# Kernel optimization log

Measured on AMD Instinct MI355X. Metric: run time of the kernel, lower is better.

Reference implementation:

```python
import jax, jax.numpy as jnp
import numpy as np

# ---- static config (mirrors GptOssDecoderLayer init) ----
H = 1024      # hidden_size
HD = 64       # head_size
NQ = 16       # num_query_heads
NKV = 4       # num_key_value_heads
G = NQ // NKV # num_key_value_groups
E = 8         # num_experts
TOPK = 2      # experts_per_token
FFN = 1024    # expert intermediate (== hidden in GPT-OSS)
B, Q = 4, 128 # batch sequences, new query tokens per sequence
P, PS = 8, 128
S = P * PS    # kv length per sequence
T = B * Q     # total query tokens
SW = 128      # sliding window (layer_idx % 2 == 0 -> active)
LIMIT = 7.0   # swiglu_limit
ALPHA = 1.702
EPS = 1e-5
NEG = -1e30
SCALE = HD ** -0.5


def rmsnorm(x, w):
    return x * w * jax.lax.rsqrt(jnp.mean(x * x, axis=-1, keepdims=True) + EPS)


def setup_inputs() -> dict:
    key = jax.random.key(0)
    ks = jax.random.split(key, 16)
    hidden = jax.random.normal(ks[0], (T, H), jnp.float32)
    kv_cache = jax.random.normal(ks[1], (B * P, 2, PS, NKV, HD), jnp.float32)
    kv_page_indices = jnp.arange(B * P, dtype=jnp.int32).reshape(B, P)
    # additive causal mask: query q sits at absolute position S - Q + q
    qpos = S - Q + jnp.arange(Q)
    kpos = jnp.arange(S)
    causal = qpos[:, None] >= kpos[None, :]
    attention_mask = jnp.broadcast_to(
        jnp.where(causal, 0.0, NEG).astype(jnp.float32), (B, Q, S))
    sinks = 0.1 * jax.random.normal(ks[2], (NQ,), jnp.float32)
    w_qkv = jax.random.normal(ks[3], (H, HD * (NQ + 2 * NKV)), jnp.float32) / np.sqrt(H)
    b_qkv = jnp.zeros((HD * (NQ + 2 * NKV),), jnp.float32)
    w_o = jax.random.normal(ks[4], (NQ * HD, H), jnp.float32) / np.sqrt(NQ * HD)
    b_o = jnp.zeros((H,), jnp.float32)
    ln1_w = jnp.ones((H,), jnp.float32)
    ln2_w = jnp.ones((H,), jnp.float32)
    w_router = jax.random.normal(ks[5], (H, E), jnp.float32) / np.sqrt(H)
    b_router = jnp.zeros((E,), jnp.float32)
    w_gate_up = jax.random.normal(ks[6], (E, H, 2 * FFN), jnp.float32) / np.sqrt(H)
    b_gate_up = jnp.zeros((E, 2 * FFN), jnp.float32)
    w_down = jax.random.normal(ks[7], (E, FFN, H), jnp.float32) / np.sqrt(FFN)
    b_down = jnp.zeros((E, H), jnp.float32)
    return dict(hidden=hidden, kv_cache=kv_cache, attention_mask=attention_mask,
                kv_page_indices=kv_page_indices, sinks=sinks, w_qkv=w_qkv,
                b_qkv=b_qkv, w_o=w_o, b_o=b_o, ln1_w=ln1_w, ln2_w=ln2_w,
                w_router=w_router, b_router=b_router, w_gate_up=w_gate_up,
                b_gate_up=b_gate_up, w_down=w_down, b_down=b_down)


def reference(hidden, kv_cache, attention_mask, kv_page_indices, sinks,
              w_qkv, b_qkv, w_o, b_o, ln1_w, ln2_w, w_router, b_router,
              w_gate_up, b_gate_up, w_down, b_down):
    # ---- attention block ----
    x = rmsnorm(hidden, ln1_w)
    qkv = x @ w_qkv + b_qkv                       # [T, HD*(NQ+2*NKV)]
    q = qkv[:, :NQ * HD].reshape(B, Q, NQ, HD)
    k_new = qkv[:, NQ * HD:(NQ + NKV) * HD].reshape(B, Q, NKV, HD)
    v_new = qkv[:, (NQ + NKV) * HD:].reshape(B, Q, NKV, HD)
    # gather paged KV cache -> [B, S, NKV, HD]; write new tokens into tail slots
    pages = kv_cache[kv_page_indices]             # [B, P, 2, PS, NKV, HD]
    K = pages[:, :, 0].reshape(B, S, NKV, HD).at[:, S - Q:].set(k_new)
    V = pages[:, :, 1].reshape(B, S, NKV, HD).at[:, S - Q:].set(v_new)
    Kr = jnp.repeat(K, G, axis=2)                 # GQA expand -> [B, S, NQ, HD]
    Vr = jnp.repeat(V, G, axis=2)
    scores = jnp.einsum('bqhd,bshd->bhqs', q * SCALE, Kr) + attention_mask[:, None]
    # sliding-window (module trims pages outside the window; equivalent mask)
    qpos = S - Q + jnp.arange(Q)
    kpos = jnp.arange(S)
    win_ok = (qpos[:, None] - kpos[None, :]) < SW
    scores = jnp.where(win_ok[None, None], scores, NEG)
    m = jnp.max(scores, axis=-1)
    m = jnp.where(jnp.isinf(m) & (m < 0), 0.0, m)
    p = jnp.exp(scores - m[..., None])            # [B, NQ, Q, S]
    # attention sink joins the softmax denominator (online-softmax correction)
    denom = jnp.sum(p, axis=-1) + jnp.exp(sinks[None, :, None] - m)
    attn = jnp.einsum('bhqs,bshd->bhqd', p, Vr) / denom[..., None]
    attn = attn.transpose(0, 2, 1, 3).reshape(T, NQ * HD)
    h = hidden + attn @ w_o + b_o
    # ---- MoE block ----
    x2 = rmsnorm(h, ln2_w)
    logits = x2 @ w_router + b_router             # [T, E]
    vals, idx = jax.lax.top_k(logits, TOPK)
    wts = jax.nn.softmax(vals, axis=-1)
    comb = jnp.sum(jax.nn.one_hot(idx, E, dtype=x2.dtype) * wts[..., None], axis=1)
    gu = jnp.einsum('th,ehf->etf', x2, w_gate_up) + b_gate_up[:, None, :]
    gate = jnp.minimum(gu[..., 0::2], LIMIT)
    up = jnp.clip(gu[..., 1::2], -LIMIT, LIMIT)
    glu = gate * jax.nn.sigmoid(gate * ALPHA)
    eo = jnp.einsum('etf,efh->eth', (up + 1.0) * glu, w_down) + b_down[:, None, :]
    moe = jnp.einsum('te,eth->th', comb, eo)
    return h + moe
```

## Files before the change

### kernel.cpp

```cpp
#include <hip/hip_runtime.h>

constexpr int H    = 1024;
constexpr int HD   = 64;
constexpr int NQ   = 16;
constexpr int NKV  = 4;
constexpr int E_   = 8;
constexpr int FFN  = 1024;
constexpr int B_   = 4;
constexpr int Q_   = 128;
constexpr int P_   = 8;
constexpr int PS   = 128;
constexpr int S_   = P_ * PS;
constexpr int T_   = B_ * Q_;
constexpr int QKV_N = HD * (NQ + 2 * NKV);
constexpr float EPS   = 1e-5f;
constexpr float ALPHA = 1.702f;
constexpr float LIMIT = 7.0f;
constexpr float SCALE = 0.125f;

constexpr int MAXROWS = 1536;

typedef __attribute__((ext_vector_type(4))) float f32x4;
typedef __attribute__((ext_vector_type(8))) short s16x8;

__device__ __forceinline__ unsigned short f2bf(float f) {
    unsigned u = __float_as_uint(f);
    u += 0x7FFFu + ((u >> 16) & 1u);
    return (unsigned short)(u >> 16);
}

__global__ __launch_bounds__(256) void repack_all_kernel(const float* __restrict__ wgu,
                                                         const float* __restrict__ wdn,
                                                         const float* __restrict__ wqkv,
                                                         const float* __restrict__ wo,
                                                         unsigned short* __restrict__ g,
                                                         unsigned short* __restrict__ u,
                                                         unsigned short* __restrict__ d,
                                                         unsigned short* __restrict__ q,
                                                         unsigned short* __restrict__ o,
                                                         int* __restrict__ cnt) {
    int idx = blockIdx.x;
    int tid = threadIdx.x;
    if (idx == 0 && tid < E_) cnt[tid] = 0;
    int lane = tid & 63;
    int kq = lane >> 4, c16 = lane & 15;
    if (idx < 4096) {
        int e = idx >> 9, rem = idx & 511;
        int nb = rem >> 3, kb = (rem & 7) * 4 + (tid >> 6);
        const float* s = wgu + ((size_t)e * 1024 + kb * 32 + kq * 8) * 2048 + 2 * (nb * 16 + c16);
        s16x8 pg, pu;
#pragma unroll
        for (int j = 0; j < 8; j++) {
            float2 v = *(const float2*)(s + (size_t)j * 2048);
            pg[j] = (short)f2bf(v.x);
            pu[j] = (short)f2bf(v.y);
        }
        size_t off = ((((size_t)e * 64 + nb) * 32 + kb) * 64 + lane) * 8;
        *(s16x8*)(g + off) = pg;
        *(s16x8*)(u + off) = pu;
    } else if (idx < 8192) {
        int i2 = idx - 4096;
        int e = i2 >> 9, rem = i2 & 511;
        int nb = rem >> 3, kb = (rem & 7) * 4 + (tid >> 6);
        const float* s = wdn + (size_t)e * FFN * H + (size_t)(kb * 32 + kq * 8) * 1024 + nb * 16 + c16;
        s16x8 p;
#pragma unroll
        for (int j = 0; j < 8; j++) p[j] = (short)f2bf(s[(size_t)j * 1024]);
        size_t off = (size_t)e * (64 * 32 * 64 * 8) + (((size_t)nb * 32 + kb) * 64 + lane) * 8;
        *(s16x8*)(d + off) = p;
    } else if (idx < 8960) {
        int i2 = idx - 8192;
        int nb = i2 >> 3, kb = (i2 & 7) * 4 + (tid >> 6);
        const float* s = wqkv + (size_t)(kb * 32 + kq * 8) * QKV_N + nb * 16 + c16;
        s16x8 p;
#pragma unroll
        for (int j = 0; j < 8; j++) p[j] = (short)f2bf(s[(size_t)j * QKV_N]);
        *(s16x8*)(q + (((size_t)nb * 32 + kb) * 64 + lane) * 8) = p;
    } else {
        int i2 = idx - 8960;
        int nb = i2 >> 3, kb = (i2 & 7) * 4 + (tid >> 6);
        const float* s = wo + (size_t)(kb * 32 + kq * 8) * H + nb * 16 + c16;
        s16x8 p;
#pragma unroll
        for (int j = 0; j < 8; j++) p[j] = (short)f2bf(s[(size_t)j * H]);
        *(s16x8*)(o + (((size_t)nb * 32 + kb) * 64 + lane) * 8) = p;
    }
}

__global__ __launch_bounds__(256) void rmsnorm_kernel(const float* __restrict__ in,
                                                      const float* __restrict__ w,
                                                      unsigned short* __restrict__ outb) {
    int t   = blockIdx.x;
    int tid = threadIdx.x;
    float4 v = ((const float4*)(in + (size_t)t * H))[tid];
    float ss = v.x * v.x + v.y * v.y + v.z * v.z + v.w * v.w;
#pragma unroll
    for (int off = 32; off; off >>= 1) ss += __shfl_down(ss, off);
    __shared__ float partial[4];
    __shared__ float s_inv;
    if ((tid & 63) == 0) partial[tid >> 6] = ss;
    __syncthreads();
    if (tid == 0)
        s_inv = rsqrtf((partial[0] + partial[1] + partial[2] + partial[3]) * (1.0f / H) + EPS);
    __syncthreads();
    float inv = s_inv;
    float4 wv = ((const float4*)w)[tid];
    ushort4 ob;
    ob.x = f2bf(v.x * wv.x * inv); ob.y = f2bf(v.y * wv.y * inv);
    ob.z = f2bf(v.z * wv.z * inv); ob.w = f2bf(v.w * wv.w * inv);
    ((ushort4*)(outb + (size_t)t * H))[tid] = ob;
}

__global__ __launch_bounds__(256) void gemm_splitk_bf16(const unsigned short* __restrict__ Abf,
                                                        const unsigned short* __restrict__ Bp,
                                                        const float* __restrict__ bias,
                                                        const float* __restrict__ resid,
                                                        float* __restrict__ C,
                                                        float* __restrict__ Cdup, int N) {
    int tid = threadIdx.x;
    int wv = tid >> 6, lane = tid & 63;
    int nb16 = blockIdx.x, mb = blockIdx.y * 64;
    int r16 = lane & 15, kq = lane >> 4;
    const unsigned short* ap = Abf + (size_t)(mb + r16) * 1024 + wv * 256 + kq * 8;
    const unsigned short* bp = Bp + (((size_t)nb16 * 32 + wv * 8) * 64 + lane) * 8;
    f32x4 acc[4] = {};
#pragma unroll 4
    for (int s = 0; s < 8; s++) {
        s16x8 af[4];
#pragma unroll
        for (int mt = 0; mt < 4; mt++)
            af[mt] = *(const s16x8*)(ap + mt * 16 * 1024 + s * 32);
        s16x8 bf = *(const s16x8*)(bp + s * 512);
#pragma unroll
        for (int mt = 0; mt < 4; mt++)
            acc[mt] = __builtin_amdgcn_mfma_f32_16x16x32_bf16(af[mt], bf, acc[mt], 0, 0, 0);
    }
    __shared__ float red[4][4][4][64];
#pragma unroll
    for (int mt = 0; mt < 4; mt++)
#pragma unroll
        for (int r = 0; r < 4; r++) red[wv][mt][r][lane] = acc[mt][r];
    __syncthreads();
    int mt = tid >> 6, li = tid & 63;
    int kq2 = li >> 4, c16 = li & 15;
    int col = nb16 * 16 + c16;
    float bcol = bias[col];
#pragma unroll
    for (int r = 0; r < 4; r++) {
        float s = red[0][mt][r][li] + red[1][mt][r][li] + red[2][mt][r][li] + red[3][mt][r][li];
        int row = mb + mt * 16 + kq2 * 4 + r;
        float v = s + bcol;
        if (resid) v += resid[(size_t)row * N + col];
        C[(size_t)row * N + col] = v;
        if (Cdup) Cdup[(size_t)row * N + col] = v;
    }
}

__global__ __launch_bounds__(256) void attn_group_kernel(const float* __restrict__ qkv,
                                                         const float* __restrict__ kv_cache,
                                                         const int* __restrict__ page_idx,
                                                         const float* __restrict__ sinks,
                                                         unsigned short* __restrict__ attn_bf) {
    int blk = blockIdx.x;
    int kvh = blk & 3;
    int q   = (blk >> 2) & 127;
    int b   = blk >> 9;
    int t   = b * Q_ + q;
    int tid = threadIdx.x;
    int s_lo = S_ - Q_ - 127 + q;

    __shared__ __align__(16) float Vs[128][64];
    __shared__ __align__(16) float qs4[4][64];
    __shared__ float pv[4][128];
    __shared__ float sD[4];

#pragma unroll
    for (int r = 0; r < 8; r++) {
        int l = r * 256 + tid;
        int key = l >> 4, c = l & 15;
        int s = s_lo + key;
        const float* vp;
        if (s < S_ - Q_) {
            int page = page_idx[b * P_ + (s >> 7)];
            vp = kv_cache + (size_t)page * 65536 + 32768 + (size_t)(s & 127) * (NKV * HD) + kvh * HD;
        } else {
            vp = qkv + (size_t)(b * Q_ + (s - (S_ - Q_))) * QKV_N + (NQ + NKV) * HD + kvh * HD;
        }
        ((float4*)Vs[key])[c] = *(const float4*)(vp + c * 4);
    }
    {
        int hh = tid >> 6, d2 = tid & 63;
        qs4[hh][d2] = qkv[(size_t)t * QKV_N + (kvh * 4 + hh) * HD + d2];
    }
    __syncthreads();

    {
        int key = tid & 127, hp = tid >> 7;
        int s = s_lo + key;
        const float* kp;
        if (s < S_ - Q_) {
            int page = page_idx[b * P_ + (s >> 7)];
            kp = kv_cache + (size_t)page * 65536 + (size_t)(s & 127) * (NKV * HD) + kvh * HD;
        } else {
            kp = qkv + (size_t)(b * Q_ + (s - (S_ - Q_))) * QKV_N + NQ * HD + kvh * HD;
        }
        const float4* kp4 = (const float4*)kp;
        const float4* q0p = (const float4*)qs4[hp * 2];
        const float4* q1p = (const float4*)qs4[hp * 2 + 1];
        float sc0 = 0.f, sc1 = 0.f;
#pragma unroll
        for (int d4 = 0; d4 < 16; d4++) {
            float4 kk = kp4[d4];
            float4 q0 = q0p[d4], q1 = q1p[d4];
            sc0 += q0.x * kk.x + q0.y * kk.y + q0.z * kk.z + q0.w * kk.w;
            sc1 += q1.x * kk.x + q1.y * kk.y + q1.z * kk.z + q1.w * kk.w;
        }
        pv[hp * 2][key]     = sc0 * SCALE;
        pv[hp * 2 + 1][key] = sc1 * SCALE;
    }
    __syncthreads();

    {
        int wv = tid >> 6, lane = tid & 63;
        float a0 = pv[wv][lane], a1 = pv[wv][lane + 64];
        float m = fmaxf(a0, a1);
#pragma unroll
        for (int off = 32; off; off >>= 1) m = fmaxf(m, __shfl_xor(m, off));
        float p0 = __expf(a0 - m), p1 = __expf(a1 - m);
        float l = p0 + p1;
#pragma unroll
        for (int off = 32; off; off >>= 1) l += __shfl_xor(l, off);
        pv[wv][lane] = p0;
        pv[wv][lane + 64] = p1;
        if (lane == 0) sD[wv] = l + __expf(sinks[kvh * 4 + wv] - m);
    }
    __syncthreads();

    {
        int hh = tid >> 6, d2 = tid & 63;
        float a0 = 0.f, a1 = 0.f, a2 = 0.f, a3 = 0.f;
#pragma unroll 4
        for (int i = 0; i < 128; i += 4) {
            a0 += pv[hh][i]     * Vs[i][d2];
            a1 += pv[hh][i + 1] * Vs[i + 1][d2];
            a2 += pv[hh][i + 2] * Vs[i + 2][d2];
            a3 += pv[hh][i + 3] * Vs[i + 3][d2];
        }
        float acc = ((a0 + a1) + (a2 + a3)) / sD[hh];
        attn_bf[(size_t)t * (NQ * HD) + (kvh * 4 + hh) * HD + d2] = f2bf(acc);
    }
}

__global__ __launch_bounds__(256) void rms_router_kernel(const float* __restrict__ hbuf,
                                                         const float* __restrict__ ln2w,
                                                         const float* __restrict__ w_router,
                                                         const float* __restrict__ b_router,
                                                         unsigned short* __restrict__ x2bf,
                                                         int* __restrict__ ridx,
                                                         float* __restrict__ rwt,
                                                         int* __restrict__ cnt) {
    int t = blockIdx.x;
    int tid = threadIdx.x;
    float4 v = ((const float4*)(hbuf + (size_t)t * H))[tid];
    float ss = v.x * v.x + v.y * v.y + v.z * v.z + v.w * v.w;
#pragma unroll
    for (int off = 32; off; off >>= 1) ss += __shfl_down(ss, off);
    __shared__ float partial[4];
    __shared__ float s_inv;
    if ((tid & 63) == 0) partial[tid >> 6] = ss;
    __syncthreads();
    if (tid == 0)
        s_inv = rsqrtf((partial[0] + partial[1] + partial[2] + partial[3]) * (1.0f / H) + EPS);
    __syncthreads();
    float inv = s_inv;
    float4 wv = ((const float4*)ln2w)[tid];
    float4 o;
    o.x = v.x * wv.x * inv; o.y = v.y * wv.y * inv;
    o.z = v.z * wv.z * inv; o.w = v.w * wv.w * inv;
    ushort4 ob;
    ob.x = f2bf(o.x); ob.y = f2bf(o.y); ob.z = f2bf(o.z); ob.w = f2bf(o.w);
    ((ushort4*)(x2bf + (size_t)t * H))[tid] = ob;

    const float4* wr = (const float4*)(w_router + (size_t)tid * 4 * E_);
    float p[E_];
    {
        float4 r0a = wr[0], r0b = wr[1];
        float4 r1a = wr[2], r1b = wr[3];
        float4 r2a = wr[4], r2b = wr[5];
        float4 r3a = wr[6], r3b = wr[7];
        p[0] = o.x * r0a.x + o.y * r1a.x + o.z * r2a.x + o.w * r3a.x;
        p[1] = o.x * r0a.y + o.y * r1a.y + o.z * r2a.y + o.w * r3a.y;
        p[2] = o.x * r0a.z + o.y * r1a.z + o.z * r2a.z + o.w * r3a.z;
        p[3] = o.x * r0a.w + o.y * r1a.w + o.z * r2a.w + o.w * r3a.w;
        p[4] = o.x * r0b.x + o.y * r1b.x + o.z * r2b.x + o.w * r3b.x;
        p[5] = o.x * r0b.y + o.y * r1b.y + o.z * r2b.y + o.w * r3b.y;
        p[6] = o.x * r0b.z + o.y * r1b.z + o.z * r2b.z + o.w * r3b.z;
        p[7] = o.x * r0b.w + o.y * r1b.w + o.z * r2b.w + o.w * r3b.w;
    }
    __shared__ float wsum[4][E_];
    int wv2 = tid >> 6, lane = tid & 63;
#pragma unroll
    for (int e = 0; e < E_; e++) {
        float r = p[e];
#pragma unroll
        for (int off = 32; off; off >>= 1) r += __shfl_xor(r, off);
        if (lane == 0) wsum[wv2][e] = r;
    }
    __syncthreads();
    __shared__ float logits[E_];
    if (tid < E_)
        logits[tid] = wsum[0][tid] + wsum[1][tid] + wsum[2][tid] + wsum[3][tid] + b_router[tid];
    __syncthreads();
    if (tid == 0) {
        int i0 = 0; float v0 = logits[0];
        for (int ee = 1; ee < E_; ee++)
            if (logits[ee] > v0) { v0 = logits[ee]; i0 = ee; }
        int i1 = -1; float v1 = -3.4e38f;
        for (int ee = 0; ee < E_; ee++)
            if (ee != i0 && logits[ee] > v1) { v1 = logits[ee]; i1 = ee; }
        float w0 = 1.0f / (1.0f + __expf(v1 - v0));
        ridx[t * 2] = i0; ridx[t * 2 + 1] = i1;
        rwt[t * 2] = w0;  rwt[t * 2 + 1] = 1.0f - w0;
        atomicAdd(&cnt[i0], 1);
        atomicAdd(&cnt[i1], 1);
    }
}

__global__ __launch_bounds__(256) void plumb_kernel(const int* __restrict__ cnt,
                                                    const int* __restrict__ ridx,
                                                    int* __restrict__ poff,
                                                    int* __restrict__ list) {
    __shared__ int lpos[E_], lpoff[E_];
    int tid = threadIdx.x;
    if (tid == 0) {
        int run = 0;
        for (int e = 0; e < E_; e++) { lpoff[e] = run; poff[e] = run; run += (cnt[e] + 63) & ~63; }
    }
    if (tid < E_) lpos[tid] = 0;
    __syncthreads();
    for (int i = tid; i < 2 * T_; i += 256) {
        int e = ridx[i];
        int pp = atomicAdd(&lpos[e], 1);
        list[lpoff[e] + pp] = i;
    }
}

__global__ __launch_bounds__(256) void moe_gateup_sk(const unsigned short* __restrict__ x2bf,
                                                     const int* __restrict__ list,
                                                     const int* __restrict__ cnt,
                                                     const int* __restrict__ poff,
                                                     const unsigned short* __restrict__ wg,
                                                     const unsigned short* __restrict__ wu,
                                                     const float* __restrict__ b_gate_up,
                                                     unsigned short* __restrict__ act_bf) {
    int e  = blockIdx.y >> 3;
    int tl = blockIdx.y & 7;
    int n  = cnt[e];
    if (tl * 128 >= n) return;
    int base = poff[e];
    int nb = blockIdx.x;

    int tid = threadIdx.x;
    int wv = tid >> 6, lane = tid & 63;
    int r16 = lane & 15, kq = lane >> 4;
    const unsigned short* ap[8];
#pragma unroll
    for (int mt = 0; mt < 8; mt++) {
        int row = tl * 128 + mt * 16 + r16;
        int t2 = (row < n) ? list[base + row] : 0;
        ap[mt] = x2bf + (size_t)(t2 >> 1) * 1024 + wv * 256 + kq * 8;
    }
    size_t boff = ((((size_t)e * 64 + nb) * 32 + wv * 8) * 64 + lane) * 8;
    const unsigned short* gp = wg + boff;
    const unsigned short* up = wu + boff;

    f32x4 accg[8] = {}, accu[8] = {};
#pragma unroll 2
    for (int s = 0; s < 8; s++) {
        s16x8 bg = *(const s16x8*)(gp + s * 512);
        s16x8 bu = *(const s16x8*)(up + s * 512);
#pragma unroll
        for (int mt = 0; mt < 8; mt++) {
            s16x8 af = *(const s16x8*)(ap[mt] + s * 32);
            accg[mt] = __builtin_amdgcn_mfma_f32_16x16x32_bf16(af, bg, accg[mt], 0, 0, 0);
            accu[mt] = __builtin_amdgcn_mfma_f32_16x16x32_bf16(af, bu, accu[mt], 0, 0, 0);
        }
    }
    __shared__ float redg[4][4][4][64];
    __shared__ float redu[4][4][4][64];
    int col = nb * 16 + (tid & 15);
    float bg_b = b_gate_up[(size_t)e * 2048 + 2 * col];
    float bu_b = b_gate_up[(size_t)e * 2048 + 2 * col + 1];
#pragma unroll
    for (int h = 0; h < 2; h++) {
        __syncthreads();
#pragma unroll
        for (int m2 = 0; m2 < 4; m2++)
#pragma unroll
            for (int r = 0; r < 4; r++) {
                redg[wv][m2][r][lane] = accg[h * 4 + m2][r];
                redu[wv][m2][r][lane] = accu[h * 4 + m2][r];
            }
        __syncthreads();
        int m2 = tid >> 6, li = tid & 63;
        int kq2 = li >> 4;
#pragma unroll
        for (int r = 0; r < 4; r++) {
            int rr = tl * 128 + (h * 4 + m2) * 16 + kq2 * 4 + r;
            if (rr < n) {
                float g = redg[0][m2][r][li] + redg[1][m2][r][li] + redg[2][m2][r][li] + redg[3][m2][r][li];
                float u = redu[0][m2][r][li] + redu[1][m2][r][li] + redu[2][m2][r][li] + redu[3][m2][r][li];
                float gate = fminf(g + bg_b, LIMIT);
                float up2 = fminf(fmaxf(u + bu_b, -LIMIT), LIMIT);
                float glu = gate / (1.0f + __expf(-ALPHA * gate));
                act_bf[(size_t)(base + rr) * FFN + col] = f2bf((up2 + 1.0f) * glu);
            }
        }
    }
}

__global__ __launch_bounds__(256) void moe_down_sk(const unsigned short* __restrict__ act_bf,
                                                   const int* __restrict__ list,
                                                   const int* __restrict__ cnt,
                                                   const int* __restrict__ poff,
                                                   const float* __restrict__ rwt,
                                                   const unsigned short* __restrict__ wd,
                                                   const float* __restrict__ b_down,
                                                   float* __restrict__ out) {
    int e  = blockIdx.y >> 3;
    int tl = blockIdx.y & 7;
    int n  = cnt[e];
    if (tl * 128 >= n) return;
    int base = poff[e];
    int nb = blockIdx.x;

    int tid = threadIdx.x;
    int wv = tid >> 6, lane = tid & 63;
    int r16 = lane & 15, kq = lane >> 4;
    const unsigned short* ap = act_bf + (size_t)(base + tl * 128 + r16) * 1024 + wv * 256 + kq * 8;
    const unsigned short* bp = wd + (size_t)e * (64 * 32 * 64 * 8) + (((size_t)nb * 32 + wv * 8) * 64 + lane) * 8;

    f32x4 acc[8] = {};
#pragma unroll 2
    for (int s = 0; s < 8; s++) {
        s16x8 bf = *(const s16x8*)(bp + s * 512);
#pragma unroll
        for (int mt = 0; mt < 8; mt++) {
            s16x8 af = *(const s16x8*)(ap + mt * 16 * 1024 + s * 32);
            acc[mt] = __builtin_amdgcn_mfma_f32_16x16x32_bf16(af, bf, acc[mt], 0, 0, 0);
        }
    }
    __shared__ float red[4][4][4][64];
    int col = nb * 16 + (tid & 15);
    float bcol = b_down[(size_t)e * 1024 + col];
#pragma unroll
    for (int h = 0; h < 2; h++) {
        __syncthreads();
#pragma unroll
        for (int m2 = 0; m2 < 4; m2++)
#pragma unroll
            for (int r = 0; r < 4; r++) red[wv][m2][r][lane] = acc[h * 4 + m2][r];
        __syncthreads();
        int m2 = tid >> 6, li = tid & 63;
        int kq2 = li >> 4;
#pragma unroll
        for (int r = 0; r < 4; r++) {
            int rr = tl * 128 + (h * 4 + m2) * 16 + kq2 * 4 + r;
            if (rr < n) {
                float s = red[0][m2][r][li] + red[1][m2][r][li] + red[2][m2][r][li] + red[3][m2][r][li];
                int t2 = list[base + rr];
                atomicAdd(&out[(size_t)(t2 >> 1) * H + col], rwt[t2] * (s + bcol));
            }
        }
    }
}

extern "C" void kernel_launch(void* const* d_in, const int* in_sizes, int n_in,
                              void* d_out, int out_size, void* d_ws, size_t ws_size,
                              hipStream_t stream) {
    const float* hidden          = (const float*)d_in[0];
    const float* kv_cache        = (const float*)d_in[1];
    const int*   kv_page_indices = (const int*)d_in[3];
    const float* sinks           = (const float*)d_in[4];
    const float* w_qkv           = (const float*)d_in[5];
    const float* b_qkv           = (const float*)d_in[6];
    const float* w_o             = (const float*)d_in[7];
    const float* b_o             = (const float*)d_in[8];
    const float* ln1_w           = (const float*)d_in[9];
    const float* ln2_w           = (const float*)d_in[10];
    const float* w_router        = (const float*)d_in[11];
    const float* b_router        = (const float*)d_in[12];
    const float* w_gate_up       = (const float*)d_in[13];
    const float* b_gate_up       = (const float*)d_in[14];
    const float* w_down          = (const float*)d_in[15];
    const float* b_down          = (const float*)d_in[16];
    float* out = (float*)d_out;

    char* base = (char*)d_ws;
    float* qkv   = (float*)base;                       base += (size_t)T_ * QKV_N * 4;
    float* hbuf  = (float*)base;                       base += (size_t)T_ * H * 4;
    unsigned short* x_bf    = (unsigned short*)base;   base += (size_t)T_ * H * 2;
    unsigned short* x2_bf   = (unsigned short*)base;   base += (size_t)T_ * H * 2;
    unsigned short* attn_bf = (unsigned short*)base;   base += (size_t)T_ * NQ * HD * 2;
    unsigned short* act_bf  = (unsigned short*)base;   base += (size_t)(MAXROWS + 128) * FFN * 2;
    unsigned short* wq_bf   = (unsigned short*)base;   base += (size_t)H * QKV_N * 2;
    unsigned short* wo_bf   = (unsigned short*)base;   base += (size_t)H * H * 2;
    unsigned short* wg_bf   = (unsigned short*)base;   base += (size_t)E_ * H * FFN * 2;
    unsigned short* wu_bf   = (unsigned short*)base;   base += (size_t)E_ * H * FFN * 2;
    unsigned short* wd_bf   = (unsigned short*)base;   base += (size_t)E_ * FFN * H * 2;
    float* rwt  = (float*)base;                        base += 2 * T_ * 4;
    int*   ridx = (int*)base;                          base += 2 * T_ * 4;
    int*   cnt  = (int*)base;                          base += E_ * 4;
    int*   poff = (int*)base;                          base += E_ * 4;
    int*   list = (int*)base;                          base += MAXROWS * 4;

    repack_all_kernel<<<9472, 256, 0, stream>>>(w_gate_up, w_down, w_qkv, w_o,
                                                wg_bf, wu_bf, wd_bf, wq_bf, wo_bf, cnt);
    rmsnorm_kernel<<<T_, 256, 0, stream>>>(hidden, ln1_w, x_bf);
    gemm_splitk_bf16<<<dim3(QKV_N / 16, T_ / 64), 256, 0, stream>>>(
        x_bf, wq_bf, b_qkv, nullptr, qkv, nullptr, QKV_N);
    attn_group_kernel<<<B_ * Q_ * NKV, 256, 0, stream>>>(qkv, kv_cache, kv_page_indices, sinks, attn_bf);
    gemm_splitk_bf16<<<dim3(H / 16, T_ / 64), 256, 0, stream>>>(
        attn_bf, wo_bf, b_o, hidden, hbuf, out, H);
    rms_router_kernel<<<T_, 256, 0, stream>>>(hbuf, ln2_w, w_router, b_router,
                                              x2_bf, ridx, rwt, cnt);
    plumb_kernel<<<1, 256, 0, stream>>>(cnt, ridx, poff, list);
    moe_gateup_sk<<<dim3(FFN / 16, E_ * 8), 256, 0, stream>>>(
        x2_bf, list, cnt, poff, wg_bf, wu_bf, b_gate_up, act_bf);
    moe_down_sk<<<dim3(H / 16, E_ * 8), 256, 0, stream>>>(
        act_bf, list, cnt, poff, rwt, wd_bf, b_down, out);
}
```

Baseline: 311.8 us.

## Drop weight repack pass; convert fp32 weights to bf16 inside GEMM loads

Removes the separate kernel that converted all fp32 weights (QKV, O, gate/up, down) into a bf16 MFMA-friendly layout each call. Each GEMM now reads the fp32 weights directly with strided per-row loads and converts them to bf16 in registers. The counter reset moves into the rmsnorm kernel. This cuts a full read-and-write pass over roughly 100MB of expert weights and one launch, but the GEMM loads are now strided scalar fp32 reads that move twice the bytes, and weight tiles reused by several M-blocks get converted again in each block.

```diff
diff --git a/kernel.cpp b/kernel.cpp
--- a/kernel.cpp
+++ b/kernel.cpp
@@ -29,69 +29,13 @@
     return (unsigned short)(u >> 16);
 }
 
-__global__ __launch_bounds__(256) void repack_all_kernel(const float* __restrict__ wgu,
-                                                         const float* __restrict__ wdn,
-                                                         const float* __restrict__ wqkv,
-                                                         const float* __restrict__ wo,
-                                                         unsigned short* __restrict__ g,
-                                                         unsigned short* __restrict__ u,
-                                                         unsigned short* __restrict__ d,
-                                                         unsigned short* __restrict__ q,
-                                                         unsigned short* __restrict__ o,
-                                                         int* __restrict__ cnt) {
-    int idx = blockIdx.x;
-    int tid = threadIdx.x;
-    if (idx == 0 && tid < E_) cnt[tid] = 0;
-    int lane = tid & 63;
-    int kq = lane >> 4, c16 = lane & 15;
-    if (idx < 4096) {
-        int e = idx >> 9, rem = idx & 511;
-        int nb = rem >> 3, kb = (rem & 7) * 4 + (tid >> 6);
-        const float* s = wgu + ((size_t)e * 1024 + kb * 32 + kq * 8) * 2048 + 2 * (nb * 16 + c16);
-        s16x8 pg, pu;
-#pragma unroll
-        for (int j = 0; j < 8; j++) {
-            float2 v = *(const float2*)(s + (size_t)j * 2048);
-            pg[j] = (short)f2bf(v.x);
-            pu[j] = (short)f2bf(v.y);
-        }
-        size_t off = ((((size_t)e * 64 + nb) * 32 + kb) * 64 + lane) * 8;
-        *(s16x8*)(g + off) = pg;
-        *(s16x8*)(u + off) = pu;
-    } else if (idx < 8192) {
-        int i2 = idx - 4096;
-        int e = i2 >> 9, rem = i2 & 511;
-        int nb = rem >> 3, kb = (rem & 7) * 4 + (tid >> 6);
-        const float* s = wdn + (size_t)e * FFN * H + (size_t)(kb * 32 + kq * 8) * 1024 + nb * 16 + c16;
-        s16x8 p;
-#pragma unroll
-        for (int j = 0; j < 8; j++) p[j] = (short)f2bf(s[(size_t)j * 1024]);
-        size_t off = (size_t)e * (64 * 32 * 64 * 8) + (((size_t)nb * 32 + kb) * 64 + lane) * 8;
-        *(s16x8*)(d + off) = p;
-    } else if (idx < 8960) {
-        int i2 = idx - 8192;
-        int nb = i2 >> 3, kb = (i2 & 7) * 4 + (tid >> 6);
-        const float* s = wqkv + (size_t)(kb * 32 + kq * 8) * QKV_N + nb * 16 + c16;
-        s16x8 p;
-#pragma unroll
-        for (int j = 0; j < 8; j++) p[j] = (short)f2bf(s[(size_t)j * QKV_N]);
-        *(s16x8*)(q + (((size_t)nb * 32 + kb) * 64 + lane) * 8) = p;
-    } else {
-        int i2 = idx - 8960;
-        int nb = i2 >> 3, kb = (i2 & 7) * 4 + (tid >> 6);
-        const float* s = wo + (size_t)(kb * 32 + kq * 8) * H + nb * 16 + c16;
-        s16x8 p;
-#pragma unroll
-        for (int j = 0; j < 8; j++) p[j] = (short)f2bf(s[(size_t)j * H]);
-        *(s16x8*)(o + (((size_t)nb * 32 + kb) * 64 + lane) * 8) = p;
-    }
-}
-
 __global__ __launch_bounds__(256) void rmsnorm_kernel(const float* __restrict__ in,
                                                       const float* __restrict__ w,
-                                                      unsigned short* __restrict__ outb) {
+                                                      unsigned short* __restrict__ outb,
+                                                      int* __restrict__ cnt) {
     int t   = blockIdx.x;
     int tid = threadIdx.x;
+    if (t == 0 && tid < E_) cnt[tid] = 0;
     float4 v = ((const float4*)(in + (size_t)t * H))[tid];
     float ss = v.x * v.x + v.y * v.y + v.z * v.z + v.w * v.w;
 #pragma unroll
@@ -111,8 +55,8 @@
     ((ushort4*)(outb + (size_t)t * H))[tid] = ob;
 }
 
-__global__ __launch_bounds__(256) void gemm_splitk_bf16(const unsigned short* __restrict__ Abf,
-                                                        const unsigned short* __restrict__ Bp,
+__global__ __launch_bounds__(256) void gemm_splitk_f32b(const unsigned short* __restrict__ Abf,
+                                                        const float* __restrict__ W,
                                                         const float* __restrict__ bias,
                                                         const float* __restrict__ resid,
                                                         float* __restrict__ C,
@@ -122,15 +66,18 @@
     int nb16 = blockIdx.x, mb = blockIdx.y * 64;
     int r16 = lane & 15, kq = lane >> 4;
     const unsigned short* ap = Abf + (size_t)(mb + r16) * 1024 + wv * 256 + kq * 8;
-    const unsigned short* bp = Bp + (((size_t)nb16 * 32 + wv * 8) * 64 + lane) * 8;
+    const float* wp = W + (size_t)(wv * 256 + kq * 8) * N + nb16 * 16 + r16;
     f32x4 acc[4] = {};
 #pragma unroll 4
     for (int s = 0; s < 8; s++) {
+        s16x8 bf;
+#pragma unroll
+        for (int j = 0; j < 8; j++)
+            bf[j] = (short)f2bf(wp[(size_t)(s * 32 + j) * N]);
         s16x8 af[4];
 #pragma unroll
         for (int mt = 0; mt < 4; mt++)
             af[mt] = *(const s16x8*)(ap + mt * 16 * 1024 + s * 32);
-        s16x8 bf = *(const s16x8*)(bp + s * 512);
 #pragma unroll
         for (int mt = 0; mt < 4; mt++)
             acc[mt] = __builtin_amdgcn_mfma_f32_16x16x32_bf16(af[mt], bf, acc[mt], 0, 0, 0);
@@ -349,8 +296,7 @@
                                                      const int* __restrict__ list,
                                                      const int* __restrict__ cnt,
                                                      const int* __restrict__ poff,
-                                                     const unsigned short* __restrict__ wg,
-                                                     const unsigned short* __restrict__ wu,
+                                                     const float* __restrict__ wgu,
                                                      const float* __restrict__ b_gate_up,
                                                      unsigned short* __restrict__ act_bf) {
     int e  = blockIdx.y >> 3;
@@ -370,15 +316,18 @@
         int t2 = (row < n) ? list[base + row] : 0;
         ap[mt] = x2bf + (size_t)(t2 >> 1) * 1024 + wv * 256 + kq * 8;
     }
-    size_t boff = ((((size_t)e * 64 + nb) * 32 + wv * 8) * 64 + lane) * 8;
-    const unsigned short* gp = wg + boff;
-    const unsigned short* up = wu + boff;
+    const float* wp = wgu + ((size_t)e * 1024 + wv * 256 + kq * 8) * 2048 + 2 * (nb * 16 + r16);
 
     f32x4 accg[8] = {}, accu[8] = {};
 #pragma unroll 2
     for (int s = 0; s < 8; s++) {
-        s16x8 bg = *(const s16x8*)(gp + s * 512);
-        s16x8 bu = *(const s16x8*)(up + s * 512);
+        s16x8 bg, bu;
+#pragma unroll
+        for (int j = 0; j < 8; j++) {
+            float2 v = *(const float2*)(wp + (size_t)(s * 32 + j) * 2048);
+            bg[j] = (short)f2bf(v.x);
+            bu[j] = (short)f2bf(v.y);
+        }
 #pragma unroll
         for (int mt = 0; mt < 8; mt++) {
             s16x8 af = *(const s16x8*)(ap[mt] + s * 32);
@@ -424,7 +373,7 @@
                                                    const int* __restrict__ cnt,
                                                    const int* __restrict__ poff,
                                                    const float* __restrict__ rwt,
-                                                   const unsigned short* __restrict__ wd,
+                                                   const float* __restrict__ wdn,
                                                    const float* __restrict__ b_down,
                                                    float* __restrict__ out) {
     int e  = blockIdx.y >> 3;
@@ -438,12 +387,15 @@
     int wv = tid >> 6, lane = tid & 63;
     int r16 = lane & 15, kq = lane >> 4;
     const unsigned short* ap = act_bf + (size_t)(base + tl * 128 + r16) * 1024 + wv * 256 + kq * 8;
-    const unsigned short* bp = wd + (size_t)e * (64 * 32 * 64 * 8) + (((size_t)nb * 32 + wv * 8) * 64 + lane) * 8;
+    const float* wp = wdn + (size_t)e * FFN * H + (size_t)(wv * 256 + kq * 8) * 1024 + nb * 16 + r16;
 
     f32x4 acc[8] = {};
 #pragma unroll 2
     for (int s = 0; s < 8; s++) {
-        s16x8 bf = *(const s16x8*)(bp + s * 512);
+        s16x8 bf;
+#pragma unroll
+        for (int j = 0; j < 8; j++)
+            bf[j] = (short)f2bf(wp[(size_t)(s * 32 + j) * 1024]);
 #pragma unroll
         for (int mt = 0; mt < 8; mt++) {
             s16x8 af = *(const s16x8*)(ap + mt * 16 * 1024 + s * 32);
@@ -503,30 +455,23 @@
     unsigned short* x2_bf   = (unsigned short*)base;   base += (size_t)T_ * H * 2;
     unsigned short* attn_bf = (unsigned short*)base;   base += (size_t)T_ * NQ * HD * 2;
     unsigned short* act_bf  = (unsigned short*)base;   base += (size_t)(MAXROWS + 128) * FFN * 2;
-    unsigned short* wq_bf   = (unsigned short*)base;   base += (size_t)H * QKV_N * 2;
-    unsigned short* wo_bf   = (unsigned short*)base;   base += (size_t)H * H * 2;
-    unsigned short* wg_bf   = (unsigned short*)base;   base += (size_t)E_ * H * FFN * 2;
-    unsigned short* wu_bf   = (unsigned short*)base;   base += (size_t)E_ * H * FFN * 2;
-    unsigned short* wd_bf   = (unsigned short*)base;   base += (size_t)E_ * FFN * H * 2;
     float* rwt  = (float*)base;                        base += 2 * T_ * 4;
     int*   ridx = (int*)base;                          base += 2 * T_ * 4;
     int*   cnt  = (int*)base;                          base += E_ * 4;
     int*   poff = (int*)base;                          base += E_ * 4;
     int*   list = (int*)base;                          base += MAXROWS * 4;
 
-    repack_all_kernel<<<9472, 256, 0, stream>>>(w_gate_up, w_down, w_qkv, w_o,
-                                                wg_bf, wu_bf, wd_bf, wq_bf, wo_bf, cnt);
-    rmsnorm_kernel<<<T_, 256, 0, stream>>>(hidden, ln1_w, x_bf);
-    gemm_splitk_bf16<<<dim3(QKV_N / 16, T_ / 64), 256, 0, stream>>>(
-        x_bf, wq_bf, b_qkv, nullptr, qkv, nullptr, QKV_N);
+    rmsnorm_kernel<<<T_, 256, 0, stream>>>(hidden, ln1_w, x_bf, cnt);
+    gemm_splitk_f32b<<<dim3(QKV_N / 16, T_ / 64), 256, 0, stream>>>(
+        x_bf, w_qkv, b_qkv, nullptr, qkv, nullptr, QKV_N);
     attn_group_kernel<<<B_ * Q_ * NKV, 256, 0, stream>>>(qkv, kv_cache, kv_page_indices, sinks, attn_bf);
-    gemm_splitk_bf16<<<dim3(H / 16, T_ / 64), 256, 0, stream>>>(
-        attn_bf, wo_bf, b_o, hidden, hbuf, out, H);
+    gemm_splitk_f32b<<<dim3(H / 16, T_ / 64), 256, 0, stream>>>(
+        attn_bf, w_o, b_o, hidden, hbuf, out, H);
     rms_router_kernel<<<T_, 256, 0, stream>>>(hbuf, ln2_w, w_router, b_router,
                                               x2_bf, ridx, rwt, cnt);
     plumb_kernel<<<1, 256, 0, stream>>>(cnt, ridx, poff, list);
     moe_gateup_sk<<<dim3(FFN / 16, E_ * 8), 256, 0, stream>>>(
-        x2_bf, list, cnt, poff, wg_bf, wu_bf, b_gate_up, act_bf);
+        x2_bf, list, cnt, poff, w_gate_up, b_gate_up, act_bf);
     moe_down_sk<<<dim3(H / 16, E_ * 8), 256, 0, stream>>>(
-        act_bf, list, cnt, poff, rwt, wd_bf, b_down, out);
-}
+        act_bf, list, cnt, poff, rwt, w_down, b_down, out);
+}
```

Measured after the change: 312.4 us. No clear change (+0.2%).
